# Kernel optimization log

Hardware: AMD Instinct MI355X
Metric: run time of the kernel (lower is better)

## Reference

```python
import jax, jax.numpy as jnp
import numpy as np

B, S, D, R, H = 32, 2048, 512, 4, 32  # batch, seq, input_dim, num_regimes, gru hidden

def setup_inputs() -> dict:
    key = jax.random.key(0)
    ks = jax.random.split(key, 16)
    def lin(k, fan_out, fan_in):
        s = 1.0 / np.sqrt(fan_in)
        kw, kb = jax.random.split(k)
        return (jax.random.uniform(kw, (fan_out, fan_in), jnp.float32, -s, s),
                jax.random.uniform(kb, (fan_out,), jnp.float32, -s, s))
    x = jax.random.normal(ks[0], (B, S, D), jnp.float32)
    rw1, rb1 = lin(ks[1], 128, D)
    rw2, rb2 = lin(ks[2], 64, 128)
    rw3, rb3 = lin(ks[3], R, 64)
    # experts stacked: [R, out, in]
    e1 = [lin(jax.random.fold_in(ks[4], i), 64, D) for i in range(R)]
    e2 = [lin(jax.random.fold_in(ks[5], i), 64, 64) for i in range(R)]
    ew1 = jnp.stack([w for w, _ in e1]); eb1 = jnp.stack([b for _, b in e1])
    ew2 = jnp.stack([w for w, _ in e2]); eb2 = jnp.stack([b for _, b in e2])
    sg = 1.0 / np.sqrt(H)
    gw_ih = jax.random.uniform(ks[6], (3 * H, R), jnp.float32, -sg, sg)
    gw_hh = jax.random.uniform(ks[7], (3 * H, H), jnp.float32, -sg, sg)
    gb_ih = jax.random.uniform(ks[8], (3 * H,), jnp.float32, -sg, sg)
    gb_hh = jax.random.uniform(ks[9], (3 * H,), jnp.float32, -sg, sg)
    return dict(x=x, rw1=rw1, rb1=rb1, rw2=rw2, rb2=rb2, rw3=rw3, rb3=rb3,
                ew1=ew1, eb1=eb1, ew2=ew2, eb2=eb2,
                gw_ih=gw_ih, gw_hh=gw_hh, gb_ih=gb_ih, gb_hh=gb_hh)

def reference(x, rw1, rb1, rw2, rb2, rw3, rb3, ew1, eb1, ew2, eb2, gw_ih, gw_hh, gb_ih, gb_hh):
    # --- router (dropout is identity in eval) ---
    h = jax.nn.relu(jnp.einsum('bsd,fd->bsf', x, rw1) + rb1)
    h = jax.nn.relu(jnp.einsum('bsf,gf->bsg', h, rw2) + rb2)
    probs = jax.nn.softmax(jnp.einsum('bsg,rg->bsr', h, rw3) + rb3, axis=-1)  # [B,S,R]
    # --- batched experts: one fused batched-GEMM instead of a python loop ---
    e = jax.nn.relu(jnp.einsum('bsd,red->bsre', x, ew1) + eb1)      # [B,S,R,64]
    e = jax.nn.relu(jnp.einsum('bsre,rfe->bsrf', e, ew2) + eb2)     # [B,S,R,64]
    weighted = jnp.einsum('bsrf,bsr->bsf', e, probs)                 # [B,S,64]
    # --- GRU over regime probs (pytorch gate ordering r,z,n) ---
    def step(hprev, xt):
        gi = xt @ gw_ih.T + gb_ih    # [B,3H]
        gh = hprev @ gw_hh.T + gb_hh
        ir, iz, inn = jnp.split(gi, 3, axis=-1)
        hr, hz, hn = jnp.split(gh, 3, axis=-1)
        r = jax.nn.sigmoid(ir + hr)
        z = jax.nn.sigmoid(iz + hz)
        n = jnp.tanh(inn + r * hn)
        hnew = (1.0 - z) * n + z * hprev
        return hnew, hnew
    h0 = jnp.zeros((probs.shape[0], gw_hh.shape[1]), probs.dtype)
    _, trans = jax.lax.scan(step, h0, jnp.swapaxes(probs, 0, 1))
    trans = jnp.swapaxes(trans, 0, 1)  # [B,S,H]
    uncertainty = jnp.std(probs, axis=-1, ddof=1)  # torch.std is unbiased
    return probs, weighted, trans, uncertainty
```

## Files before the change

### kernel.cpp

```cpp
#include <hip/hip_runtime.h>
#include <math.h>

#define NTOK 65536
#define TOK 64
#define NTILE 1024

__global__ __launch_bounds__(256, 2) void k_router(
    const float* __restrict__ x,
    const float* __restrict__ rw1, const float* __restrict__ rb1,
    const float* __restrict__ rw2, const float* __restrict__ rb2,
    const float* __restrict__ rw3, const float* __restrict__ rb3,
    float* __restrict__ probs_out, float* __restrict__ unc_out)
{
    __shared__ float XsT[32][68];
    __shared__ float WsT[32][132];
    __shared__ float H1[64][132];
    __shared__ float H2[64][68];

    const int tid = threadIdx.x;
    const int tx = tid & 15, ty = tid >> 4;
    const long t0 = (long)blockIdx.x * TOK;

    float acc[4][8];
#pragma unroll
    for (int i = 0; i < 4; i++)
#pragma unroll
        for (int o = 0; o < 8; o++) acc[i][o] = 0.f;

    for (int kc = 0; kc < 16; kc++) {
        __syncthreads();
#pragma unroll
        for (int s = 0; s < 2; s++) {
            int id = tid + s * 256;
            int tok = id >> 3, kq = id & 7;
            float4 v = *(const float4*)&x[(t0 + tok) * 512 + kc * 32 + kq * 4];
            XsT[kq * 4 + 0][tok] = v.x; XsT[kq * 4 + 1][tok] = v.y;
            XsT[kq * 4 + 2][tok] = v.z; XsT[kq * 4 + 3][tok] = v.w;
        }
#pragma unroll
        for (int s = 0; s < 4; s++) {
            int id = tid + s * 256;
            int out = id >> 3, kq = id & 7;
            float4 v = *(const float4*)&rw1[(long)out * 512 + kc * 32 + kq * 4];
            WsT[kq * 4 + 0][out] = v.x; WsT[kq * 4 + 1][out] = v.y;
            WsT[kq * 4 + 2][out] = v.z; WsT[kq * 4 + 3][out] = v.w;
        }
        __syncthreads();
#pragma unroll
        for (int k = 0; k < 32; k++) {
            const float4 xv = *(const float4*)&XsT[k][ty * 4];
            const float4 wa = *(const float4*)&WsT[k][tx * 4];
            const float4 wb = *(const float4*)&WsT[k][64 + tx * 4];
            const float xs[4] = {xv.x, xv.y, xv.z, xv.w};
            const float ws[8] = {wa.x, wa.y, wa.z, wa.w, wb.x, wb.y, wb.z, wb.w};
#pragma unroll
            for (int i = 0; i < 4; i++)
#pragma unroll
                for (int o = 0; o < 8; o++)
                    acc[i][o] = fmaf(xs[i], ws[o], acc[i][o]);
        }
    }

#pragma unroll
    for (int o = 0; o < 8; o++) {
        const int col = (o < 4) ? (tx * 4 + o) : (64 + tx * 4 + (o - 4));
        float b = rb1[col];
#pragma unroll
        for (int i = 0; i < 4; i++) {
            float v = acc[i][o] + b;
            H1[ty * 4 + i][col] = v > 0.f ? v : 0.f;
        }
    }
    __syncthreads();

    float a2[4][4];
#pragma unroll
    for (int i = 0; i < 4; i++)
#pragma unroll
        for (int o = 0; o < 4; o++) a2[i][o] = 0.f;

    for (int k4 = 0; k4 < 32; k4++) {
        float4 hv[4], wv[4];
#pragma unroll
        for (int i = 0; i < 4; i++) hv[i] = *(const float4*)&H1[ty * 4 + i][k4 * 4];
#pragma unroll
        for (int o = 0; o < 4; o++) wv[o] = *(const float4*)&rw2[(tx * 4 + o) * 128 + k4 * 4];
#pragma unroll
        for (int i = 0; i < 4; i++)
#pragma unroll
            for (int o = 0; o < 4; o++)
                a2[i][o] += hv[i].x * wv[o].x + hv[i].y * wv[o].y +
                            hv[i].z * wv[o].z + hv[i].w * wv[o].w;
    }
#pragma unroll
    for (int o = 0; o < 4; o++) {
        float b = rb2[tx * 4 + o];
#pragma unroll
        for (int i = 0; i < 4; i++) {
            float v = a2[i][o] + b;
            H2[ty * 4 + i][tx * 4 + o] = v > 0.f ? v : 0.f;
        }
    }
    __syncthreads();

    if (tid < 64) {
        int tok = tid;
        float lg[4];
#pragma unroll
        for (int r = 0; r < 4; r++) {
            float s = rb3[r];
            for (int k4 = 0; k4 < 16; k4++) {
                float4 h = *(const float4*)&H2[tok][k4 * 4];
                float4 w = *(const float4*)&rw3[r * 64 + k4 * 4];
                s += h.x * w.x + h.y * w.y + h.z * w.z + h.w * w.w;
            }
            lg[r] = s;
        }
        float m = fmaxf(fmaxf(lg[0], lg[1]), fmaxf(lg[2], lg[3]));
        float e0 = __expf(lg[0] - m), e1 = __expf(lg[1] - m);
        float e2 = __expf(lg[2] - m), e3 = __expf(lg[3] - m);
        float inv = __builtin_amdgcn_rcpf(e0 + e1 + e2 + e3);
        float p0 = e0 * inv, p1 = e1 * inv, p2 = e2 * inv, p3 = e3 * inv;
        *(float4*)&probs_out[(t0 + tok) * 4] = make_float4(p0, p1, p2, p3);
        float mean = 0.25f * (p0 + p1 + p2 + p3);
        float d0 = p0 - mean, d1 = p1 - mean, d2 = p2 - mean, d3 = p3 - mean;
        unc_out[t0 + tok] = sqrtf((d0 * d0 + d1 * d1 + d2 * d2 + d3 * d3) * (1.f / 3.f));
    }
}

__global__ __launch_bounds__(256, 2) void k_experts_gru(
    const float* __restrict__ x,
    const float* __restrict__ ew1, const float* __restrict__ eb1,
    const float* __restrict__ ew2, const float* __restrict__ eb2,
    const float* __restrict__ probs, float* __restrict__ weighted_out,
    const float* __restrict__ gwih, const float* __restrict__ gwhh,
    const float* __restrict__ gbih, const float* __restrict__ gbhh,
    float* __restrict__ trans_out)
{
    if (blockIdx.x < 32) {
        if (threadIdx.x >= 64) return;
        const int b = blockIdx.x;
        const int l = threadIdx.x;
        const int j = l & 31, half = l >> 5;
        __shared__ float hS[32];

        float whh[3][16];
#pragma unroll
        for (int g = 0; g < 3; g++) {
            const float* wp = gwhh + (j + 32 * g) * 32 + half * 16;
#pragma unroll
            for (int q = 0; q < 4; q++) {
                float4 w = *(const float4*)(wp + q * 4);
                whh[g][q * 4 + 0] = w.x; whh[g][q * 4 + 1] = w.y;
                whh[g][q * 4 + 2] = w.z; whh[g][q * 4 + 3] = w.w;
            }
        }
        float wih[3][4];
#pragma unroll
        for (int g = 0; g < 3; g++) {
            float4 w = *(const float4*)&gwih[(j + 32 * g) * 4];
            wih[g][0] = w.x; wih[g][1] = w.y; wih[g][2] = w.z; wih[g][3] = w.w;
        }
        const float bR = gbih[j] + gbhh[j];
        const float bZ = gbih[j + 32] + gbhh[j + 32];
        const float bIN = gbih[j + 64], bHN = gbhh[j + 64];

        const float* pb = probs + (long)b * 2048 * 4;
        float4 p0 = *(const float4*)pb;
        float4 p1 = *(const float4*)(pb + 4);
        float hk[16];
#pragma unroll
        for (int k = 0; k < 16; k++) hk[k] = 0.f;
        float hj = 0.f;
        float* tr = trans_out + (long)b * 2048 * 32 + j;

        for (int t = 0; t < 2048; t++) {
            const int tn = (t + 2 < 2047) ? (t + 2) : 2047;
            float4 p2 = *(const float4*)(pb + tn * 4);

            float aR0 = 0.f, aR1 = 0.f, aZ0 = 0.f, aZ1 = 0.f, aN0 = 0.f, aN1 = 0.f;
#pragma unroll
            for (int k = 0; k < 16; k += 2) {
                aR0 = fmaf(whh[0][k],     hk[k],     aR0);
                aR1 = fmaf(whh[0][k + 1], hk[k + 1], aR1);
                aZ0 = fmaf(whh[1][k],     hk[k],     aZ0);
                aZ1 = fmaf(whh[1][k + 1], hk[k + 1], aZ1);
                aN0 = fmaf(whh[2][k],     hk[k],     aN0);
                aN1 = fmaf(whh[2][k + 1], hk[k + 1], aN1);
            }
            float aR = aR0 + aR1, aZ = aZ0 + aZ1, aN = aN0 + aN1;
            aR += __shfl_xor(aR, 32);
            aZ += __shfl_xor(aZ, 32);
            aN += __shfl_xor(aN, 32);

            float giR = fmaf(wih[0][3], p0.w, fmaf(wih[0][2], p0.z,
                        fmaf(wih[0][1], p0.y, fmaf(wih[0][0], p0.x, bR))));
            float giZ = fmaf(wih[1][3], p0.w, fmaf(wih[1][2], p0.z,
                        fmaf(wih[1][1], p0.y, fmaf(wih[1][0], p0.x, bZ))));
            float giN = fmaf(wih[2][3], p0.w, fmaf(wih[2][2], p0.z,
                        fmaf(wih[2][1], p0.y, fmaf(wih[2][0], p0.x, bIN))));

            float r = __builtin_amdgcn_rcpf(1.f + __expf(-(giR + aR)));
            float z = __builtin_amdgcn_rcpf(1.f + __expf(-(giZ + aZ)));
            float nx = giN + r * (aN + bHN);
            float n = fmaf(2.f, __builtin_amdgcn_rcpf(1.f + __expf(-2.f * nx)), -1.f);
            hj = fmaf(z, hj - n, n);

            if (l < 32) tr[t * 32] = hj;
            hS[j] = hj;
            asm volatile("s_waitcnt lgkmcnt(0)" ::: "memory");
#pragma unroll
            for (int q = 0; q < 4; q++) {
                float4 h4 = *(const float4*)&hS[half * 16 + q * 4];
                hk[q * 4 + 0] = h4.x; hk[q * 4 + 1] = h4.y;
                hk[q * 4 + 2] = h4.z; hk[q * 4 + 3] = h4.w;
            }
            p0 = p1; p1 = p2;
        }
        return;
    }

    __shared__ float XsT[32][68];
    __shared__ float WsT[32][132];
    __shared__ float E1[64][132];
    __shared__ float pS[64][4];

    const int tid = threadIdx.x;
    const int tx = tid & 15, ty = tid >> 4;
    const long t0 = (long)(blockIdx.x - 32) * TOK;

    if (tid < 64) *(float4*)&pS[tid][0] = *(const float4*)&probs[(t0 + tid) * 4];

    float wacc[4][8];
#pragma unroll
    for (int i = 0; i < 4; i++)
#pragma unroll
        for (int o = 0; o < 8; o++) wacc[i][o] = 0.f;

    for (int g = 0; g < 2; g++) {
        float acc[4][8];
#pragma unroll
        for (int i = 0; i < 4; i++)
#pragma unroll
            for (int o = 0; o < 8; o++) acc[i][o] = 0.f;

        for (int kc = 0; kc < 16; kc++) {
            __syncthreads();
#pragma unroll
            for (int s = 0; s < 2; s++) {
                int id = tid + s * 256;
                int tok = id >> 3, kq = id & 7;
                float4 v = *(const float4*)&x[(t0 + tok) * 512 + kc * 32 + kq * 4];
                XsT[kq * 4 + 0][tok] = v.x; XsT[kq * 4 + 1][tok] = v.y;
                XsT[kq * 4 + 2][tok] = v.z; XsT[kq * 4 + 3][tok] = v.w;
            }
#pragma unroll
            for (int s = 0; s < 4; s++) {
                int id = tid + s * 256;
                int out = id >> 3, kq = id & 7;
                float4 v = *(const float4*)&ew1[(long)(g * 128 + out) * 512 + kc * 32 + kq * 4];
                WsT[kq * 4 + 0][out] = v.x; WsT[kq * 4 + 1][out] = v.y;
                WsT[kq * 4 + 2][out] = v.z; WsT[kq * 4 + 3][out] = v.w;
            }
            __syncthreads();
#pragma unroll
            for (int k = 0; k < 32; k++) {
                const float4 xv = *(const float4*)&XsT[k][ty * 4];
                const float4 wa = *(const float4*)&WsT[k][tx * 4];
                const float4 wb = *(const float4*)&WsT[k][64 + tx * 4];
                const float xs[4] = {xv.x, xv.y, xv.z, xv.w};
                const float ws[8] = {wa.x, wa.y, wa.z, wa.w, wb.x, wb.y, wb.z, wb.w};
#pragma unroll
                for (int i = 0; i < 4; i++)
#pragma unroll
                    for (int o = 0; o < 8; o++)
                        acc[i][o] = fmaf(xs[i], ws[o], acc[i][o]);
            }
        }
        __syncthreads();
#pragma unroll
        for (int o = 0; o < 8; o++) {
            const int col = (o < 4) ? (tx * 4 + o) : (64 + tx * 4 + (o - 4));
            float b = eb1[g * 128 + col];
#pragma unroll
            for (int i = 0; i < 4; i++) {
                float v = acc[i][o] + b;
                E1[ty * 4 + i][col] = v > 0.f ? v : 0.f;
            }
        }
        __syncthreads();

        const int rl = tx >> 3;
        const int fb = (tx & 7) * 8;
        const int rg = g * 2 + rl;

        float a2[4][8];
#pragma unroll
        for (int i = 0; i < 4; i++)
#pragma unroll
            for (int o = 0; o < 8; o++) a2[i][o] = 0.f;

        for (int k4 = 0; k4 < 16; k4++) {
            float4 hv[4];
#pragma unroll
            for (int i = 0; i < 4; i++)
                hv[i] = *(const float4*)&E1[ty * 4 + i][rl * 64 + k4 * 4];
#pragma unroll
            for (int o = 0; o < 8; o++) {
                float4 wv = *(const float4*)&ew2[(long)(rg * 64 + fb + o) * 64 + k4 * 4];
#pragma unroll
                for (int i = 0; i < 4; i++)
                    a2[i][o] += hv[i].x * wv.x + hv[i].y * wv.y +
                                hv[i].z * wv.z + hv[i].w * wv.w;
            }
        }
        float pr[4];
#pragma unroll
        for (int i = 0; i < 4; i++) pr[i] = pS[ty * 4 + i][rg];
#pragma unroll
        for (int o = 0; o < 8; o++) {
            float b = eb2[rg * 64 + fb + o];
#pragma unroll
            for (int i = 0; i < 4; i++) {
                float v = a2[i][o] + b;
                v = v > 0.f ? v : 0.f;
                wacc[i][o] = fmaf(pr[i], v, wacc[i][o]);
            }
        }
        __syncthreads();
    }

#pragma unroll
    for (int i = 0; i < 4; i++)
#pragma unroll
        for (int o = 0; o < 8; o++)
            wacc[i][o] += __shfl_xor(wacc[i][o], 8);

    if ((tx & 8) == 0) {
#pragma unroll
        for (int i = 0; i < 4; i++) {
            float4 v0 = make_float4(wacc[i][0], wacc[i][1], wacc[i][2], wacc[i][3]);
            float4 v1 = make_float4(wacc[i][4], wacc[i][5], wacc[i][6], wacc[i][7]);
            long base = (t0 + ty * 4 + i) * 64 + (tx & 7) * 8;
            *(float4*)&weighted_out[base] = v0;
            *(float4*)&weighted_out[base + 4] = v1;
        }
    }
}

extern "C" void kernel_launch(void* const* d_in, const int* in_sizes, int n_in,
                              void* d_out, int out_size, void* d_ws, size_t ws_size,
                              hipStream_t stream) {
    const float* x    = (const float*)d_in[0];
    const float* rw1  = (const float*)d_in[1];
    const float* rb1  = (const float*)d_in[2];
    const float* rw2  = (const float*)d_in[3];
    const float* rb2  = (const float*)d_in[4];
    const float* rw3  = (const float*)d_in[5];
    const float* rb3  = (const float*)d_in[6];
    const float* ew1  = (const float*)d_in[7];
    const float* eb1  = (const float*)d_in[8];
    const float* ew2  = (const float*)d_in[9];
    const float* eb2  = (const float*)d_in[10];
    const float* gwih = (const float*)d_in[11];
    const float* gwhh = (const float*)d_in[12];
    const float* gbih = (const float*)d_in[13];
    const float* gbhh = (const float*)d_in[14];

    float* out        = (float*)d_out;
    float* probs_o    = out;
    float* weighted_o = out + 262144;
    float* trans_o    = out + 262144 + 4194304;
    float* unc_o      = trans_o + 2097152;

    hipLaunchKernelGGL(k_router, dim3(NTILE), dim3(256), 0, stream,
                       x, rw1, rb1, rw2, rb2, rw3, rb3, probs_o, unc_o);
    hipLaunchKernelGGL(k_experts_gru, dim3(NTILE + 32), dim3(256), 0, stream,
                       x, ew1, eb1, ew2, eb2, probs_o, weighted_o,
                       gwih, gwhh, gbih, gbhh, trans_o);
}
```

Measured before the change: 818.5 us.

## Broadcast GRU hidden state via DPP and permlane32 swaps instead of LDS

The sequential GRU recurrence now shares the hidden state across lanes with DPP row permutations and permlane32_swap instead of an LDS write, a waitcnt and vector reads. Each lane computes the full 32-wide dot product from XOR-permuted weight copies, which removes the cross-half shuffle reduction. The goal is to shorten the per-timestep latency of the serial 2048-step chain. In exchange it doubles the per-lane FMA work and weight registers and adds about 30 cross-lane ops per step.

```diff
diff --git a/kernel.cpp b/kernel.cpp
--- a/kernel.cpp
+++ b/kernel.cpp
@@ -4,6 +4,9 @@
 #define NTOK 65536
 #define TOK 64
 #define NTILE 1024
+
+#define DPPMOV(v, ctrl) \
+    ((unsigned)__builtin_amdgcn_update_dpp(0, (int)(v), (ctrl), 0xF, 0xF, true))
 
 __global__ __launch_bounds__(256, 2) void k_router(
     const float* __restrict__ x,
@@ -141,18 +144,18 @@
         if (threadIdx.x >= 64) return;
         const int b = blockIdx.x;
         const int l = threadIdx.x;
-        const int j = l & 31, half = l >> 5;
-        __shared__ float hS[32];
-
-        float whh[3][16];
+        const int i = l & 15;
+        const int sOwn = (l >> 5) & 1;
+        const int j = i | (sOwn << 4);
+
+        float wA[3][16], wB[3][16];
 #pragma unroll
         for (int g = 0; g < 3; g++) {
-            const float* wp = gwhh + (j + 32 * g) * 32 + half * 16;
-#pragma unroll
-            for (int q = 0; q < 4; q++) {
-                float4 w = *(const float4*)(wp + q * 4);
-                whh[g][q * 4 + 0] = w.x; whh[g][q * 4 + 1] = w.y;
-                whh[g][q * 4 + 2] = w.z; whh[g][q * 4 + 3] = w.w;
+            const float* row = gwhh + (j + 32 * g) * 32;
+#pragma unroll
+            for (int p = 0; p < 16; p++) {
+                wA[g][p] = row[sOwn * 16 + (i ^ p)];
+                wB[g][p] = row[(1 - sOwn) * 16 + (i ^ p)];
             }
         }
         float wih[3][4];
@@ -165,33 +168,45 @@
         const float bZ = gbih[j + 32] + gbhh[j + 32];
         const float bIN = gbih[j + 64], bHN = gbhh[j + 64];
 
+        unsigned lid = (unsigned)l;
+        auto rt = __builtin_amdgcn_permlane32_swap(lid, lid, false, false);
+        const bool r0_own = ((unsigned)rt[0] == lid);
+
+        float hA[16], hB[16];
+#pragma unroll
+        for (int p = 0; p < 16; p++) { hA[p] = 0.f; hB[p] = 0.f; }
+        float hj = 0.f;
+
         const float* pb = probs + (long)b * 2048 * 4;
         float4 p0 = *(const float4*)pb;
         float4 p1 = *(const float4*)(pb + 4);
-        float hk[16];
-#pragma unroll
-        for (int k = 0; k < 16; k++) hk[k] = 0.f;
-        float hj = 0.f;
         float* tr = trans_out + (long)b * 2048 * 32 + j;
+        const bool writer = ((l & 16) == 0);
 
         for (int t = 0; t < 2048; t++) {
-            const int tn = (t + 2 < 2047) ? (t + 2) : 2047;
+            const int tn = (t + 2 < 2048) ? (t + 2) : 2047;
             float4 p2 = *(const float4*)(pb + tn * 4);
 
-            float aR0 = 0.f, aR1 = 0.f, aZ0 = 0.f, aZ1 = 0.f, aN0 = 0.f, aN1 = 0.f;
-#pragma unroll
-            for (int k = 0; k < 16; k += 2) {
-                aR0 = fmaf(whh[0][k],     hk[k],     aR0);
-                aR1 = fmaf(whh[0][k + 1], hk[k + 1], aR1);
-                aZ0 = fmaf(whh[1][k],     hk[k],     aZ0);
-                aZ1 = fmaf(whh[1][k + 1], hk[k + 1], aZ1);
-                aN0 = fmaf(whh[2][k],     hk[k],     aN0);
-                aN1 = fmaf(whh[2][k + 1], hk[k + 1], aN1);
-            }
-            float aR = aR0 + aR1, aZ = aZ0 + aZ1, aN = aN0 + aN1;
-            aR += __shfl_xor(aR, 32);
-            aZ += __shfl_xor(aZ, 32);
-            aN += __shfl_xor(aN, 32);
+            float cR0 = 0.f, cR1 = 0.f, cZ0 = 0.f, cZ1 = 0.f, cN0 = 0.f, cN1 = 0.f;
+            float dR0 = 0.f, dR1 = 0.f, dZ0 = 0.f, dZ1 = 0.f, dN0 = 0.f, dN1 = 0.f;
+#pragma unroll
+            for (int p = 0; p < 16; p += 2) {
+                cR0 = fmaf(wA[0][p],     hA[p],     cR0);
+                cR1 = fmaf(wA[0][p + 1], hA[p + 1], cR1);
+                cZ0 = fmaf(wA[1][p],     hA[p],     cZ0);
+                cZ1 = fmaf(wA[1][p + 1], hA[p + 1], cZ1);
+                cN0 = fmaf(wA[2][p],     hA[p],     cN0);
+                cN1 = fmaf(wA[2][p + 1], hA[p + 1], cN1);
+                dR0 = fmaf(wB[0][p],     hB[p],     dR0);
+                dR1 = fmaf(wB[0][p + 1], hB[p + 1], dR1);
+                dZ0 = fmaf(wB[1][p],     hB[p],     dZ0);
+                dZ1 = fmaf(wB[1][p + 1], hB[p + 1], dZ1);
+                dN0 = fmaf(wB[2][p],     hB[p],     dN0);
+                dN1 = fmaf(wB[2][p + 1], hB[p + 1], dN1);
+            }
+            float dotR = (cR0 + cR1) + (dR0 + dR1);
+            float dotZ = (cZ0 + cZ1) + (dZ0 + dZ1);
+            float dotN = (cN0 + cN1) + (dN0 + dN1);
 
             float giR = fmaf(wih[0][3], p0.w, fmaf(wih[0][2], p0.z,
                         fmaf(wih[0][1], p0.y, fmaf(wih[0][0], p0.x, bR))));
@@ -200,21 +215,40 @@
             float giN = fmaf(wih[2][3], p0.w, fmaf(wih[2][2], p0.z,
                         fmaf(wih[2][1], p0.y, fmaf(wih[2][0], p0.x, bIN))));
 
-            float r = __builtin_amdgcn_rcpf(1.f + __expf(-(giR + aR)));
-            float z = __builtin_amdgcn_rcpf(1.f + __expf(-(giZ + aZ)));
-            float nx = giN + r * (aN + bHN);
+            float r = __builtin_amdgcn_rcpf(1.f + __expf(-(giR + dotR)));
+            float z = __builtin_amdgcn_rcpf(1.f + __expf(-(giZ + dotZ)));
+            float nx = giN + r * (dotN + bHN);
             float n = fmaf(2.f, __builtin_amdgcn_rcpf(1.f + __expf(-2.f * nx)), -1.f);
             hj = fmaf(z, hj - n, n);
 
-            if (l < 32) tr[t * 32] = hj;
-            hS[j] = hj;
-            asm volatile("s_waitcnt lgkmcnt(0)" ::: "memory");
-#pragma unroll
-            for (int q = 0; q < 4; q++) {
-                float4 h4 = *(const float4*)&hS[half * 16 + q * 4];
-                hk[q * 4 + 0] = h4.x; hk[q * 4 + 1] = h4.y;
-                hk[q * 4 + 2] = h4.z; hk[q * 4 + 3] = h4.w;
-            }
+            if (writer) tr[t * 32] = hj;
+
+            unsigned h0 = __builtin_bit_cast(unsigned, hj);
+            unsigned v1  = DPPMOV(h0, 0xB1);
+            unsigned v2  = DPPMOV(h0, 0x4E);
+            unsigned v3  = DPPMOV(v1, 0x4E);
+            unsigned v7  = DPPMOV(h0, 0x141);
+            unsigned v6  = DPPMOV(v1, 0x141);
+            unsigned v5  = DPPMOV(v2, 0x141);
+            unsigned v4  = DPPMOV(v3, 0x141);
+            unsigned v15 = DPPMOV(h0, 0x140);
+            unsigned v14 = DPPMOV(v1, 0x140);
+            unsigned v13 = DPPMOV(v2, 0x140);
+            unsigned v12 = DPPMOV(v3, 0x140);
+            unsigned v11 = DPPMOV(v4, 0x140);
+            unsigned v10 = DPPMOV(v5, 0x140);
+            unsigned v9  = DPPMOV(v6, 0x140);
+            unsigned v8  = DPPMOV(v7, 0x140);
+            unsigned tv[16] = {h0, v1, v2, v3, v4, v5, v6, v7,
+                               v8, v9, v10, v11, v12, v13, v14, v15};
+#pragma unroll
+            for (int p = 0; p < 16; p++) {
+                auto rp = __builtin_amdgcn_permlane32_swap(tv[p], tv[p], false, false);
+                unsigned partner = r0_own ? (unsigned)rp[1] : (unsigned)rp[0];
+                hA[p] = __builtin_bit_cast(float, tv[p]);
+                hB[p] = __builtin_bit_cast(float, partner);
+            }
+
             p0 = p1; p1 = p2;
         }
         return;
```

Result: slower. 1.125 ms (+37.5%).
